# Performance work log

Measured on AMD Instinct MI355X. Metric: run time of the kernel, lower is better.

Reference implementation:

```python
import jax, jax.numpy as jnp
import numpy as np

K = 8            # hard-attention top-k neighbors per node
NEG_SLOPE = 0.2  # leaky relu slope


def setup_inputs() -> dict:
    key = jax.random.key(0)
    k1, k2, k3, k4, k5, k6 = jax.random.split(key, 6)
    N, D, F = 50000, 64, 256
    H, O = 8, 32
    feat = jax.random.normal(k1, (N, F), dtype=jnp.float32)
    neighbors = jax.random.randint(k2, (N, D), 0, N)  # src node ids per dst
    # learned params (xavier-normal-ish scale)
    p = jax.random.normal(k3, (1, F), dtype=jnp.float32) * float(np.sqrt(2.0 / (1 + F)))
    W = jax.random.normal(k4, (F, H * O), dtype=jnp.float32) * float(np.sqrt(2.0 / (F + H * O)))
    attn_l = jax.random.normal(k5, (1, H, O), dtype=jnp.float32) * float(np.sqrt(2.0 / (H * O + 1)))
    attn_r = jax.random.normal(k6, (1, H, O), dtype=jnp.float32) * float(np.sqrt(2.0 / (H * O + 1)))
    return {"feat": feat, "neighbors": neighbors, "p": p, "W": W,
            "attn_l": attn_l, "attn_r": attn_r}


def reference(feat, neighbors, p, W, attn_l, attn_r):
    N, F = feat.shape
    H, O = attn_l.shape[1], attn_l.shape[2]
    # node projection score y = |p . x| / ||p||
    y = jnp.abs(feat @ p[0]) / jnp.linalg.norm(p)          # [N]
    # hard top-k neighbor selection by source score (select_topk on 'y')
    ys = y[neighbors]                                       # [N, D]
    _, idx = jax.lax.top_k(ys, K)                           # [N, K]
    src = jnp.take_along_axis(neighbors, idx, axis=1)       # [N, K] source ids
    # gating + projection
    gate = jax.nn.sigmoid(y) * 2.0                          # [N]
    ft = ((gate[:, None] * feat) @ W).reshape(N, H, O)      # [N, H, O]
    el = jnp.sum(ft * attn_l, axis=-1)                      # [N, H]
    er = jnp.sum(ft * attn_r, axis=-1)                      # [N, H]
    # edge scores: u_add_v, leaky_relu, edge_softmax over each dst's K edges
    e = el[src] + er[:, None, :]                            # [N, K, H]
    e = jnp.where(e > 0, e, NEG_SLOPE * e)
    a = jax.nn.softmax(e, axis=1)                           # [N, K, H]
    # u_mul_e + sum aggregation
    rst = jnp.einsum('nkh,nkho->nho', a, ft[src])           # [N, H, O]
    return jax.nn.elu(rst)
```

## Files before the change

### kernel.cpp

```cpp
#include <hip/hip_runtime.h>
#include <math.h>

#define NEG_SLOPE 0.2f

typedef _Float16 half8 __attribute__((ext_vector_type(8)));
typedef _Float16 half2v __attribute__((ext_vector_type(2)));
typedef float floatx4 __attribute__((ext_vector_type(4)));

__device__ __forceinline__ float dot4f(float4 a, float4 b) {
    return a.x * b.x + a.y * b.y + a.z * b.z + a.w * b.w;
}

static __device__ __forceinline__ unsigned short f2h(float x) {
    _Float16 h = (_Float16)x;
    return __builtin_bit_cast(unsigned short, h);
}
static __device__ __forceinline__ float h2f(unsigned short u) {
    _Float16 h = __builtin_bit_cast(_Float16, u);
    return (float)h;
}

__global__ void k_prepw(const float* __restrict__ W,
                        const float* __restrict__ al,
                        const float* __restrict__ ar,
                        unsigned short* __restrict__ Wtp,
                        unsigned short* __restrict__ Mp) {
    const int k = threadIdx.x;
    if (blockIdx.x < 256) {
        const int c = blockIdx.x;
        float v = W[(size_t)k * 256 + c];
        Wtp[(size_t)(c >> 4) * 4096 + (k >> 3) * 128 + (c & 15) * 8 + (k & 7)] = f2h(v);
    } else {
        const int t = blockIdx.x - 256;
        float v = 0.f;
        if (t < 8) {
            if ((k >> 5) == t) v = al[t * 32 + (k & 31)];
        } else {
            if ((k >> 5) == (t - 8)) v = ar[(t - 8) * 32 + (k & 31)];
        }
        Mp[(k >> 3) * 128 + t * 8 + (k & 7)] = f2h(v);
    }
}

__global__ __launch_bounds__(256) void k_fused(const float4* __restrict__ feat4,
                                               const float4* __restrict__ p4,
                                               const unsigned short* __restrict__ Wtp,
                                               const unsigned short* __restrict__ Mp,
                                               float* __restrict__ y,
                                               unsigned short* __restrict__ fth,
                                               float* __restrict__ el,
                                               float* __restrict__ er,
                                               int N) {
    __shared__ unsigned short As[32][264];
    const int lane = threadIdx.x & 63;
    const int w = threadIdx.x >> 6;
    const int l16 = lane & 15, quad = lane >> 4;
    const int nb = blockIdx.x * 32;

    const float4 p = p4[lane];
    float pp = dot4f(p, p);
#pragma unroll
    for (int off = 32; off; off >>= 1) pp += __shfl_xor(pp, off, 64);
    const float rnorm = 1.0f / sqrtf(pp);

#pragma unroll
    for (int j = 0; j < 8; ++j) {
        const int m = w * 8 + j;
        int n = nb + m;
        const bool valid = n < N;
        if (!valid) n = N - 1;
        float4 f = feat4[(size_t)n * 64 + lane];
        float dp = dot4f(f, p);
#pragma unroll
        for (int off = 32; off; off >>= 1) dp += __shfl_xor(dp, off, 64);
        float yv = fabsf(dp) * rnorm;
        if (lane == 0 && valid) y[n] = yv;
        float g = 2.0f / (1.0f + __expf(-yv));
        ushort4 u;
        u.x = f2h(g * f.x);
        u.y = f2h(g * f.y);
        u.z = f2h(g * f.z);
        u.w = f2h(g * f.w);
        *(ushort4*)&As[m][lane * 4] = u;
    }
    __syncthreads();

    floatx4 acc[2][4];
#pragma unroll
    for (int mt = 0; mt < 2; ++mt)
#pragma unroll
        for (int ct = 0; ct < 4; ++ct) acc[mt][ct] = (floatx4){0.f, 0.f, 0.f, 0.f};

    const unsigned short* bbase = Wtp + (size_t)(w * 4) * 4096 + quad * 128 + l16 * 8;

    for (int ks = 0; ks < 256; ks += 32) {
        half8 a0 = *(const half8*)&As[l16][ks + quad * 8];
        half8 a1 = *(const half8*)&As[16 + l16][ks + quad * 8];
        const unsigned short* bk = bbase + (ks >> 3) * 128;
        half8 b0 = *(const half8*)(bk);
        half8 b1 = *(const half8*)(bk + 4096);
        half8 b2 = *(const half8*)(bk + 8192);
        half8 b3 = *(const half8*)(bk + 12288);
        acc[0][0] = __builtin_amdgcn_mfma_f32_16x16x32_f16(a0, b0, acc[0][0], 0, 0, 0);
        acc[0][1] = __builtin_amdgcn_mfma_f32_16x16x32_f16(a0, b1, acc[0][1], 0, 0, 0);
        acc[0][2] = __builtin_amdgcn_mfma_f32_16x16x32_f16(a0, b2, acc[0][2], 0, 0, 0);
        acc[0][3] = __builtin_amdgcn_mfma_f32_16x16x32_f16(a0, b3, acc[0][3], 0, 0, 0);
        acc[1][0] = __builtin_amdgcn_mfma_f32_16x16x32_f16(a1, b0, acc[1][0], 0, 0, 0);
        acc[1][1] = __builtin_amdgcn_mfma_f32_16x16x32_f16(a1, b1, acc[1][1], 0, 0, 0);
        acc[1][2] = __builtin_amdgcn_mfma_f32_16x16x32_f16(a1, b2, acc[1][2], 0, 0, 0);
        acc[1][3] = __builtin_amdgcn_mfma_f32_16x16x32_f16(a1, b3, acc[1][3], 0, 0, 0);
    }

    __syncthreads();
#pragma unroll
    for (int mt = 0; mt < 2; ++mt)
#pragma unroll
        for (int ct = 0; ct < 4; ++ct)
#pragma unroll
            for (int i = 0; i < 4; ++i) {
                int row = mt * 16 + quad * 4 + i;
                int col = w * 64 + ct * 16 + l16;
                unsigned short h = f2h(acc[mt][ct][i]);
                As[row][col] = h;
                int grow = nb + row;
                if (grow < N) fth[(size_t)grow * 256 + col] = h;
            }
    __syncthreads();

    if (w < 2) {
        floatx4 d = (floatx4){0.f, 0.f, 0.f, 0.f};
        for (int ks = 0; ks < 256; ks += 32) {
            half8 a = *(const half8*)&As[w * 16 + l16][ks + quad * 8];
            half8 b = *(const half8*)(Mp + (ks >> 3) * 128 + quad * 128 + l16 * 8);
            d = __builtin_amdgcn_mfma_f32_16x16x32_f16(a, b, d, 0, 0, 0);
        }
#pragma unroll
        for (int i = 0; i < 4; ++i) {
            int row = nb + w * 16 + quad * 4 + i;
            if (row < N) {
                if (l16 < 8) el[(size_t)row * 8 + l16] = d[i];
                else         er[(size_t)row * 8 + (l16 - 8)] = d[i];
            }
        }
    }
}

__global__ __launch_bounds__(256) void k_aggr(const int* __restrict__ nbr,
                                              const float* __restrict__ y,
                                              const uint2* __restrict__ fth2,
                                              const float* __restrict__ el,
                                              const float* __restrict__ er,
                                              floatx4* __restrict__ out4,
                                              int N) {
    const int lane = threadIdx.x & 63;
    const int n = blockIdx.x * 4 + (threadIdx.x >> 6);
    if (n >= N) return;
    const int h = lane >> 3;

    const int s = nbr[(size_t)n * 64 + lane];
    const unsigned int key = __float_as_uint(y[s]);

    unsigned int t = 0u;
#pragma unroll
    for (int b = 30; b >= 0; --b) {
        unsigned int cand = t | (1u << b);
        unsigned long long m = __ballot(key >= cand);
        if (__popcll(m) >= 8) t = cand;
    }
    const unsigned long long gtmask = __ballot(key > t);
    const int ngt = __popcll(gtmask);
    const unsigned long long eqmask = __ballot(key == t);
    const unsigned long long below = (1ull << lane) - 1ull;
    const int eqrank = __popcll(eqmask & below);
    const bool in8 = (key > t) | ((key == t) & (eqrank < 8 - ngt));
    unsigned long long selmask = __ballot(in8);

    int srck[8];
#pragma unroll
    for (int k = 0; k < 8; ++k) {
        int l = __ffsll((long long)selmask) - 1;
        srck[k] = __shfl(s, l, 64);
        selmask &= selmask - 1ull;
    }

    uint2 vk[8];
#pragma unroll
    for (int k = 0; k < 8; ++k) vk[k] = fth2[(size_t)srck[k] * 64 + lane];

    const float erv = er[(size_t)n * 8 + h];
    float e[8];
#pragma unroll
    for (int k = 0; k < 8; ++k) {
        float ev = el[(size_t)srck[k] * 8 + h] + erv;
        e[k] = ev > 0.f ? ev : NEG_SLOPE * ev;
    }

    float m = e[0];
#pragma unroll
    for (int k = 1; k < 8; ++k) m = fmaxf(m, e[k]);
    float sum = 0.f;
#pragma unroll
    for (int k = 0; k < 8; ++k) {
        e[k] = __expf(e[k] - m);
        sum += e[k];
    }
    const float inv = 1.0f / sum;

    half2v acc0 = (half2v){(_Float16)0, (_Float16)0};
    half2v acc1 = acc0;
#pragma unroll
    for (int k = 0; k < 8; ++k) {
        _Float16 ah = (_Float16)(e[k] * inv);
        half2v a2 = {ah, ah};
        acc0 += a2 * __builtin_bit_cast(half2v, vk[k].x);
        acc1 += a2 * __builtin_bit_cast(half2v, vk[k].y);
    }
    floatx4 r;
    r[0] = (float)acc0[0];
    r[1] = (float)acc0[1];
    r[2] = (float)acc1[0];
    r[3] = (float)acc1[1];
    r[0] = r[0] > 0.f ? r[0] : __expf(r[0]) - 1.f;
    r[1] = r[1] > 0.f ? r[1] : __expf(r[1]) - 1.f;
    r[2] = r[2] > 0.f ? r[2] : __expf(r[2]) - 1.f;
    r[3] = r[3] > 0.f ? r[3] : __expf(r[3]) - 1.f;
    __builtin_nontemporal_store(r, &out4[(size_t)n * 64 + lane]);
}

extern "C" void kernel_launch(void* const* d_in, const int* in_sizes, int n_in,
                              void* d_out, int out_size, void* d_ws, size_t ws_size,
                              hipStream_t stream) {
    const float* feat = (const float*)d_in[0];
    const int* nbr    = (const int*)d_in[1];
    const float* p    = (const float*)d_in[2];
    const float* W    = (const float*)d_in[3];
    const float* al   = (const float*)d_in[4];
    const float* ar   = (const float*)d_in[5];

    const int N = in_sizes[0] / 256;

    float* y = (float*)d_ws;
    unsigned short* Wtp = (unsigned short*)(y + N);
    unsigned short* Mp  = Wtp + 256 * 256;
    float* el = (float*)(Mp + 32 * 128);
    float* er = el + (size_t)N * 8;
    unsigned short* fth = (unsigned short*)(er + (size_t)N * 8);

    k_prepw<<<272, 256, 0, stream>>>(W, al, ar, Wtp, Mp);
    k_fused<<<(N + 31) / 32, 256, 0, stream>>>((const float4*)feat, (const float4*)p,
                                               Wtp, Mp, y, fth, el, er, N);
    k_aggr<<<(N + 3) / 4, 256, 0, stream>>>(nbr, y, (const uint2*)fth, el, er,
                                            (floatx4*)d_out, N);
}
```

Measured before the change: 171.7 us.

## Fold attention vectors into W and split scoring from the projection GEMM

Precomputes W·attn_l and W·attn_r as 16 extra weight columns, so el/er come out of the main GEMM instead of a second MFMA pass over the stored projection. Splits the fused kernel into a per-node scoring kernel and a GEMM kernel. The scoring kernel writes gated fp16 features in the MFMA tile layout, and the GEMM overwrites that buffer in place with the projected features. el/er are now stored in fp16, halving their gather traffic in aggregation. The cost is an extra global round trip for the fp16 activations and lower el/er precision.

After: 184.1 us. 7.2% more time.

```diff
diff --git a/kernel.cpp b/kernel.cpp
--- a/kernel.cpp
+++ b/kernel.cpp
@@ -10,7 +10,6 @@
 __device__ __forceinline__ float dot4f(float4 a, float4 b) {
     return a.x * b.x + a.y * b.y + a.z * b.z + a.w * b.w;
 }
-
 static __device__ __forceinline__ unsigned short f2h(float x) {
     _Float16 h = (_Float16)x;
     return __builtin_bit_cast(unsigned short, h);
@@ -20,87 +19,91 @@
     return (float)h;
 }
 
-__global__ void k_prepw(const float* __restrict__ W,
-                        const float* __restrict__ al,
-                        const float* __restrict__ ar,
-                        unsigned short* __restrict__ Wtp,
-                        unsigned short* __restrict__ Mp) {
+__global__ void k_prep(const float* __restrict__ W,
+                       const float* __restrict__ al,
+                       const float* __restrict__ ar,
+                       unsigned short* __restrict__ Wtp) {
     const int k = threadIdx.x;
     if (blockIdx.x < 256) {
         const int c = blockIdx.x;
-        float v = W[(size_t)k * 256 + c];
-        Wtp[(size_t)(c >> 4) * 4096 + (k >> 3) * 128 + (c & 15) * 8 + (k & 7)] = f2h(v);
+        Wtp[(size_t)(c >> 4) * 4096 + (k >> 3) * 128 + (c & 15) * 8 + (k & 7)] =
+            f2h(W[(size_t)k * 256 + c]);
     } else {
         const int t = blockIdx.x - 256;
-        float v = 0.f;
-        if (t < 8) {
-            if ((k >> 5) == t) v = al[t * 32 + (k & 31)];
-        } else {
-            if ((k >> 5) == (t - 8)) v = ar[(t - 8) * 32 + (k & 31)];
-        }
-        Mp[(k >> 3) * 128 + t * 8 + (k & 7)] = f2h(v);
-    }
-}
-
-__global__ __launch_bounds__(256) void k_fused(const float4* __restrict__ feat4,
+        const float* att = (t < 8) ? al : ar;
+        const int h = (t < 8) ? t : t - 8;
+        float s = 0.f;
+        for (int o = 0; o < 32; ++o) s += W[(size_t)k * 256 + h * 32 + o] * att[h * 32 + o];
+        Wtp[(size_t)16 * 4096 + (k >> 3) * 128 + t * 8 + (k & 7)] = f2h(s);
+    }
+}
+
+__global__ __launch_bounds__(256) void k_score(const float4* __restrict__ feat4,
                                                const float4* __restrict__ p4,
-                                               const unsigned short* __restrict__ Wtp,
-                                               const unsigned short* __restrict__ Mp,
                                                float* __restrict__ y,
-                                               unsigned short* __restrict__ fth,
-                                               float* __restrict__ el,
-                                               float* __restrict__ er,
+                                               unsigned short* __restrict__ Ahp,
                                                int N) {
-    __shared__ unsigned short As[32][264];
+    const int lane = threadIdx.x & 63;
+    const int n = blockIdx.x * 4 + (threadIdx.x >> 6);
+    if (n >= N) return;
+    float4 f = feat4[(size_t)n * 64 + lane];
+    float4 p = p4[lane];
+    float dp = dot4f(f, p);
+    float pp = dot4f(p, p);
+#pragma unroll
+    for (int off = 32; off; off >>= 1) {
+        dp += __shfl_xor(dp, off, 64);
+        pp += __shfl_xor(pp, off, 64);
+    }
+    float yv = fabsf(dp) / sqrtf(pp);
+    if (lane == 0) y[n] = yv;
+    float g = 2.0f / (1.0f + __expf(-yv));
+    ushort4 u;
+    u.x = f2h(g * f.x);
+    u.y = f2h(g * f.y);
+    u.z = f2h(g * f.z);
+    u.w = f2h(g * f.w);
+    const int P = n >> 4, m = n & 15;
+    size_t off = (size_t)P * 4096 + (lane >> 1) * 128 + m * 8 + (lane & 1) * 4;
+    *(ushort4*)(Ahp + off) = u;
+}
+
+__global__ __launch_bounds__(256) void k_gemm(const unsigned short* Ahp,
+                                              const unsigned short* __restrict__ Wtp,
+                                              unsigned short* fth,
+                                              unsigned short* __restrict__ elh,
+                                              unsigned short* __restrict__ erh,
+                                              int N) {
     const int lane = threadIdx.x & 63;
     const int w = threadIdx.x >> 6;
     const int l16 = lane & 15, quad = lane >> 4;
-    const int nb = blockIdx.x * 32;
-
-    const float4 p = p4[lane];
-    float pp = dot4f(p, p);
-#pragma unroll
-    for (int off = 32; off; off >>= 1) pp += __shfl_xor(pp, off, 64);
-    const float rnorm = 1.0f / sqrtf(pp);
-
-#pragma unroll
-    for (int j = 0; j < 8; ++j) {
-        const int m = w * 8 + j;
-        int n = nb + m;
-        const bool valid = n < N;
-        if (!valid) n = N - 1;
-        float4 f = feat4[(size_t)n * 64 + lane];
-        float dp = dot4f(f, p);
-#pragma unroll
-        for (int off = 32; off; off >>= 1) dp += __shfl_xor(dp, off, 64);
-        float yv = fabsf(dp) * rnorm;
-        if (lane == 0 && valid) y[n] = yv;
-        float g = 2.0f / (1.0f + __expf(-yv));
-        ushort4 u;
-        u.x = f2h(g * f.x);
-        u.y = f2h(g * f.y);
-        u.z = f2h(g * f.z);
-        u.w = f2h(g * f.w);
-        *(ushort4*)&As[m][lane * 4] = u;
-    }
-    __syncthreads();
+    const int n0 = blockIdx.x * 32;
+    const int P0 = n0 >> 4;
+    const int P1 = (n0 + 16 < N) ? P0 + 1 : P0;
 
     floatx4 acc[2][4];
-#pragma unroll
-    for (int mt = 0; mt < 2; ++mt)
+    floatx4 acce[2];
+#pragma unroll
+    for (int mt = 0; mt < 2; ++mt) {
+        acce[mt] = (floatx4){0.f, 0.f, 0.f, 0.f};
 #pragma unroll
         for (int ct = 0; ct < 4; ++ct) acc[mt][ct] = (floatx4){0.f, 0.f, 0.f, 0.f};
-
-    const unsigned short* bbase = Wtp + (size_t)(w * 4) * 4096 + quad * 128 + l16 * 8;
-
+    }
+
+    const unsigned short* abase0 = Ahp + (size_t)P0 * 4096 + quad * 128 + l16 * 8;
+    const unsigned short* abase1 = Ahp + (size_t)P1 * 4096 + quad * 128 + l16 * 8;
+    const unsigned short* bbase  = Wtp + (size_t)(w * 4) * 4096 + quad * 128 + l16 * 8;
+    const unsigned short* ebase  = Wtp + (size_t)16 * 4096 + quad * 128 + l16 * 8;
+
+#pragma unroll
     for (int ks = 0; ks < 256; ks += 32) {
-        half8 a0 = *(const half8*)&As[l16][ks + quad * 8];
-        half8 a1 = *(const half8*)&As[16 + l16][ks + quad * 8];
-        const unsigned short* bk = bbase + (ks >> 3) * 128;
-        half8 b0 = *(const half8*)(bk);
-        half8 b1 = *(const half8*)(bk + 4096);
-        half8 b2 = *(const half8*)(bk + 8192);
-        half8 b3 = *(const half8*)(bk + 12288);
+        const int ko = (ks >> 3) * 128;
+        half8 a0 = *(const half8*)(abase0 + ko);
+        half8 a1 = *(const half8*)(abase1 + ko);
+        half8 b0 = *(const half8*)(bbase + ko);
+        half8 b1 = *(const half8*)(bbase + ko + 4096);
+        half8 b2 = *(const half8*)(bbase + ko + 8192);
+        half8 b3 = *(const half8*)(bbase + ko + 12288);
         acc[0][0] = __builtin_amdgcn_mfma_f32_16x16x32_f16(a0, b0, acc[0][0], 0, 0, 0);
         acc[0][1] = __builtin_amdgcn_mfma_f32_16x16x32_f16(a0, b1, acc[0][1], 0, 0, 0);
         acc[0][2] = __builtin_amdgcn_mfma_f32_16x16x32_f16(a0, b2, acc[0][2], 0, 0, 0);
@@ -109,47 +112,45 @@
         acc[1][1] = __builtin_amdgcn_mfma_f32_16x16x32_f16(a1, b1, acc[1][1], 0, 0, 0);
         acc[1][2] = __builtin_amdgcn_mfma_f32_16x16x32_f16(a1, b2, acc[1][2], 0, 0, 0);
         acc[1][3] = __builtin_amdgcn_mfma_f32_16x16x32_f16(a1, b3, acc[1][3], 0, 0, 0);
+        if (w == 3) {
+            half8 be = *(const half8*)(ebase + ko);
+            acce[0] = __builtin_amdgcn_mfma_f32_16x16x32_f16(a0, be, acce[0], 0, 0, 0);
+            acce[1] = __builtin_amdgcn_mfma_f32_16x16x32_f16(a1, be, acce[1], 0, 0, 0);
+        }
     }
 
     __syncthreads();
+
 #pragma unroll
     for (int mt = 0; mt < 2; ++mt)
 #pragma unroll
         for (int ct = 0; ct < 4; ++ct)
 #pragma unroll
             for (int i = 0; i < 4; ++i) {
-                int row = mt * 16 + quad * 4 + i;
-                int col = w * 64 + ct * 16 + l16;
-                unsigned short h = f2h(acc[mt][ct][i]);
-                As[row][col] = h;
-                int grow = nb + row;
-                if (grow < N) fth[(size_t)grow * 256 + col] = h;
+                int row = n0 + mt * 16 + quad * 4 + i;
+                if (row < N)
+                    fth[(size_t)row * 256 + (w * 4 + ct) * 16 + l16] = f2h(acc[mt][ct][i]);
             }
-    __syncthreads();
-
-    if (w < 2) {
-        floatx4 d = (floatx4){0.f, 0.f, 0.f, 0.f};
-        for (int ks = 0; ks < 256; ks += 32) {
-            half8 a = *(const half8*)&As[w * 16 + l16][ks + quad * 8];
-            half8 b = *(const half8*)(Mp + (ks >> 3) * 128 + quad * 128 + l16 * 8);
-            d = __builtin_amdgcn_mfma_f32_16x16x32_f16(a, b, d, 0, 0, 0);
-        }
-#pragma unroll
-        for (int i = 0; i < 4; ++i) {
-            int row = nb + w * 16 + quad * 4 + i;
-            if (row < N) {
-                if (l16 < 8) el[(size_t)row * 8 + l16] = d[i];
-                else         er[(size_t)row * 8 + (l16 - 8)] = d[i];
+    if (w == 3) {
+#pragma unroll
+        for (int mt = 0; mt < 2; ++mt)
+#pragma unroll
+            for (int i = 0; i < 4; ++i) {
+                int row = n0 + mt * 16 + quad * 4 + i;
+                if (row < N) {
+                    unsigned short v = f2h(acce[mt][i]);
+                    if (l16 < 8) elh[(size_t)row * 8 + l16] = v;
+                    else         erh[(size_t)row * 8 + (l16 - 8)] = v;
+                }
             }
-        }
     }
 }
 
 __global__ __launch_bounds__(256) void k_aggr(const int* __restrict__ nbr,
                                               const float* __restrict__ y,
                                               const uint2* __restrict__ fth2,
-                                              const float* __restrict__ el,
-                                              const float* __restrict__ er,
+                                              const unsigned short* __restrict__ elh,
+                                              const unsigned short* __restrict__ erh,
                                               floatx4* __restrict__ out4,
                                               int N) {
     const int lane = threadIdx.x & 63;
@@ -187,11 +188,11 @@
 #pragma unroll
     for (int k = 0; k < 8; ++k) vk[k] = fth2[(size_t)srck[k] * 64 + lane];
 
-    const float erv = er[(size_t)n * 8 + h];
+    const float erv = h2f(erh[(size_t)n * 8 + h]);
     float e[8];
 #pragma unroll
     for (int k = 0; k < 8; ++k) {
-        float ev = el[(size_t)srck[k] * 8 + h] + erv;
+        float ev = h2f(elh[(size_t)srck[k] * 8 + h]) + erv;
         e[k] = ev > 0.f ? ev : NEG_SLOPE * ev;
     }
 
@@ -241,14 +242,15 @@
 
     float* y = (float*)d_ws;
     unsigned short* Wtp = (unsigned short*)(y + N);
-    unsigned short* Mp  = Wtp + 256 * 256;
-    float* el = (float*)(Mp + 32 * 128);
-    float* er = el + (size_t)N * 8;
-    unsigned short* fth = (unsigned short*)(er + (size_t)N * 8);
-
-    k_prepw<<<272, 256, 0, stream>>>(W, al, ar, Wtp, Mp);
-    k_fused<<<(N + 31) / 32, 256, 0, stream>>>((const float4*)feat, (const float4*)p,
-                                               Wtp, Mp, y, fth, el, er, N);
-    k_aggr<<<(N + 3) / 4, 256, 0, stream>>>(nbr, y, (const uint2*)fth, el, er,
+    unsigned short* elh = Wtp + 17 * 4096;
+    unsigned short* erh = elh + (size_t)N * 8;
+    unsigned short* Ahp = erh + (size_t)N * 8;
+
+    k_prep<<<272, 256, 0, stream>>>(W, al, ar, Wtp);
+    k_score<<<(N + 3) / 4, 256, 0, stream>>>((const float4*)feat, (const float4*)p,
+                                             y, Ahp, N);
+    k_gemm<<<(N + 31) / 32, 256, 0, stream>>>(Ahp, Wtp, Ahp ,
+                                              elh, erh, N);
+    k_aggr<<<(N + 3) / 4, 256, 0, stream>>>(nbr, y, (const uint2*)Ahp, elh, erh,
                                             (floatx4*)d_out, N);
 }
```
